# Kernel tuning notes

Measured on AMD Instinct MI355X. Metric: run time of the kernel, lower is better.

Reference implementation:

```python
import jax, jax.numpy as jnp
import numpy as np

NH, HD, WS, LL, SR, HF = 8, 32, 3, 9, 8, 682


def _ln(x, w, b, eps=1e-5):
    m = x.mean(-1, keepdims=True)
    v = ((x - m) ** 2).mean(-1, keepdims=True)
    return (x - m) * jax.lax.rsqrt(v + eps) * w + b


def _l2norm(x, eps=1e-12):
    n = jnp.sqrt(jnp.sum(x * x, axis=-1, keepdims=True))
    return x / jnp.maximum(n, eps)


def setup_inputs() -> dict:
    key = jax.random.key(0)
    ks = jax.random.split(key, 32)
    f32 = jnp.float32
    rn = lambda i, shp, s=0.02: jax.random.normal(ks[i], shp, f32) * s
    B, N, C, T = 8, 3136, 256, 1024
    d = {}
    d['x'] = jax.random.normal(ks[0], (B, N, C), f32)
    d['relative_coords_table'] = jax.random.uniform(ks[1], (T, 2), f32, minval=-1.0, maxval=1.0)
    d['seq_length_scale'] = jnp.ones((1,), f32)
    d['norm1_w'] = jnp.ones((C,), f32); d['norm1_b'] = jnp.zeros((C,), f32)
    d['q_w'] = rn(2, (C, C)); d['q_b'] = rn(3, (C,))
    d['kv_w'] = rn(4, (2 * C, C)); d['kv_b'] = rn(5, (2 * C,))
    d['temperature'] = jnp.full((NH, 1, 1), np.log(np.expm1(1.0 / 0.24)), f32)
    d['query_embedding'] = rn(6, (NH, 1, HD))
    d['relative_pos_bias_local'] = rn(7, (NH, LL), 0.0004)
    d['learnable_tokens'] = rn(8, (NH, HD, LL))
    d['learnable_bias'] = jnp.zeros((NH, 1, LL), f32)
    d['sr_w'] = rn(9, (C, C)); d['sr_b'] = rn(10, (C,))
    d['normp_w'] = jnp.ones((C,), f32); d['normp_b'] = jnp.zeros((C,), f32)
    d['cpb_fc1_w'] = rn(11, (512, 2)); d['cpb_fc1_b'] = rn(12, (512,))
    d['cpb_fc2_w'] = rn(13, (NH, 512)); d['cpb_fc2_b'] = rn(14, (NH,))
    d['proj_w'] = rn(15, (C, C)); d['proj_b'] = rn(16, (C,))
    d['norm2_w'] = jnp.ones((C,), f32); d['norm2_b'] = jnp.zeros((C,), f32)
    d['fc1_w'] = rn(17, (2 * HF, C)); d['fc1_b'] = rn(18, (2 * HF,))
    d['dw_w'] = rn(19, (HF, 1, 3, 3)); d['dw_b'] = rn(20, (HF,))
    d['fc2_w'] = rn(21, (C, HF)); d['fc2_b'] = rn(22, (C,))
    d['relative_pos_index'] = jax.random.randint(ks[23], (N, 49), 0, T)
    d['padding_mask'] = jnp.zeros((N, LL), bool)
    d['H'] = 56
    d['W'] = 56
    return d


def _forward(x, relative_coords_table, seq_length_scale, norm1_w, norm1_b, q_w, q_b, kv_w, kv_b,
             temperature, query_embedding, relative_pos_bias_local, learnable_tokens, learnable_bias,
             sr_w, sr_b, normp_w, normp_b, cpb_fc1_w, cpb_fc1_b, cpb_fc2_w, cpb_fc2_b,
             proj_w, proj_b, norm2_w, norm2_b, fc1_w, fc1_b, dw_w, dw_b, fc2_w, fc2_b,
             relative_pos_index, padding_mask, H, W):
    B, N, C = x.shape
    pH, pW = H // SR, W // SR
    pl = pH * pW
    xn = _ln(x, norm1_w, norm1_b)
    # queries: [B, nh, N, hd], cosine-normalized
    q = (xn @ q_w.T + q_b).reshape(B, N, NH, HD).transpose(0, 2, 1, 3)
    q_norm = _l2norm(q)
    q_scaled = (q_norm + query_embedding) * jax.nn.softplus(temperature) * seq_length_scale
    # local keys/values via unfold (3x3 windows, zero-padded)
    kv = xn @ kv_w.T + kv_b                                   # [B, N, 2C]
    k_l, v_l = jnp.split(kv, 2, axis=-1)
    k_l = _l2norm(k_l.reshape(B, N, NH, HD)).reshape(B, N, C)
    kvl = jnp.concatenate([k_l, v_l], -1).transpose(0, 2, 1).reshape(B, 2 * C, H, W)
    pad = WS // 2
    kvp = jnp.pad(kvl, ((0, 0), (0, 0), (pad, pad), (pad, pad)))
    wins = jnp.stack([kvp[:, :, i:i + H, j:j + W] for i in range(WS) for j in range(WS)], axis=2)
    wins = wins.reshape(B, 2 * NH, HD, LL, N).transpose(0, 1, 4, 2, 3)  # [B, 2nh, N, hd, ll]
    k_loc, v_loc = jnp.split(wins, 2, axis=1)
    attn_local = jnp.einsum('bhnd,bhndl->bhnl', q_scaled, k_loc) + relative_pos_bias_local[None, :, None, :]
    attn_local = jnp.where(padding_mask[None, None], -jnp.inf, attn_local)
    # pooled global branch
    x_ = xn.transpose(0, 2, 1).reshape(B, C, H, W)
    x_ = jax.nn.gelu(jnp.einsum('oc,bchw->bohw', sr_w, x_) + sr_b[None, :, None, None], approximate=False)
    x_ = x_.reshape(B, C, pH, SR, pW, SR).mean(axis=(3, 5))  # adaptive avg pool
    x_ = _ln(x_.reshape(B, C, pl).transpose(0, 2, 1), normp_w, normp_b)
    kvp2 = (x_ @ kv_w.T + kv_b).reshape(B, pl, 2 * NH, HD).transpose(0, 2, 1, 3)
    k_pool, v_pool = jnp.split(kvp2, 2, axis=1)               # [B, nh, pl, hd]
    cpb = jax.nn.relu(relative_coords_table @ cpb_fc1_w.T + cpb_fc1_b) @ cpb_fc2_w.T + cpb_fc2_b
    pool_bias = cpb.T[:, relative_pos_index.reshape(-1)].reshape(NH, N, pl)
    attn_pool = q_scaled @ _l2norm(k_pool).transpose(0, 1, 3, 2) + pool_bias[None]
    # joint softmax over local + pool scores
    attn = jax.nn.softmax(jnp.concatenate([attn_local, attn_pool], -1), axis=-1)
    a_loc, a_pool = attn[..., :LL], attn[..., LL:]
    x_local = jnp.einsum('bhnl,bhndl->bhnd',
                         jnp.einsum('bhnd,hdl->bhnl', q_norm, learnable_tokens) + learnable_bias[None] + a_loc,
                         v_loc)
    x_pool = a_pool @ v_pool
    out = (x_local + x_pool).transpose(0, 2, 1, 3).reshape(B, N, C)
    x = x + (out @ proj_w.T + proj_b)
    # ConvolutionalGLU MLP
    xn2 = _ln(x, norm2_w, norm2_b)
    h = xn2 @ fc1_w.T + fc1_b
    h1, v = jnp.split(h, 2, -1)
    hc = h1.transpose(0, 2, 1).reshape(B, HF, H, W)
    hc = jax.lax.conv_general_dilated(hc, dw_w, (1, 1), 'SAME', feature_group_count=HF,
                                      dimension_numbers=('NCHW', 'OIHW', 'NCHW')) + dw_b[None, :, None, None]
    h1 = hc.reshape(B, HF, N).transpose(0, 2, 1)
    h = jax.nn.gelu(h1, approximate=False) * v
    return x + (h @ fc2_w.T + fc2_b)


def reference(x, relative_coords_table, seq_length_scale, norm1_w, norm1_b, q_w, q_b, kv_w, kv_b,
              temperature, query_embedding, relative_pos_bias_local, learnable_tokens, learnable_bias,
              sr_w, sr_b, normp_w, normp_b, cpb_fc1_w, cpb_fc1_b, cpb_fc2_w, cpb_fc2_b,
              proj_w, proj_b, norm2_w, norm2_b, fc1_w, fc1_b, dw_w, dw_b, fc2_w, fc2_b,
              relative_pos_index, padding_mask, H, W):
    return _forward(x, relative_coords_table, seq_length_scale, norm1_w, norm1_b, q_w, q_b, kv_w, kv_b,
                    temperature, query_embedding, relative_pos_bias_local, learnable_tokens, learnable_bias,
                    sr_w, sr_b, normp_w, normp_b, cpb_fc1_w, cpb_fc1_b, cpb_fc2_w, cpb_fc2_b,
                    proj_w, proj_b, norm2_w, norm2_b, fc1_w, fc1_b, dw_w, dw_b, fc2_w, fc2_b,
                    relative_pos_index, padding_mask, H, W)
```

## Files before the change

### kernel.cpp

```cpp
#include <hip/hip_runtime.h>
#include <math.h>

#define B_   8
#define N_   3136
#define C_   256
#define NH_  8
#define HD_  32
#define LL_  9
#define PL_  49
#define HF_  682
#define HH   56
#define WW   56
#define MROWS (B_*N_)
#define HGLD  704
#define F2LD  704
#define HBLD  1368

typedef short          bf16x8 __attribute__((ext_vector_type(8)));
typedef unsigned short u16x8  __attribute__((ext_vector_type(8)));
typedef float          f32x4  __attribute__((ext_vector_type(4)));
typedef unsigned short u16;

static __device__ __forceinline__ float gelu_f(float x){ return 0.5f*x*(1.0f+erff(x*0.70710678118654752f)); }
static __device__ __forceinline__ u16 f2bf(float f){
// ... 121 lines not shown

  const int Kt = (K + 31) & ~31;
  const int l15 = lane & 15, quad = lane >> 4;
  int r  = tid >> 2;
  int c8 = (tid & 3) * 8;

  for (int k0=0; k0<Kt; k0+=32){
    int gk = k0 + c8;
    u16x8 av = (u16x8){0,0,0,0,0,0,0,0};
    if (m0 + r < M && gk + 8 <= lda)
      av = *(const u16x8*)(A + (size_t)(m0+r)*lda + gk);
    *(u16x8*)(&As[r*LDT + c8]) = av;
    u16x8 bv = (u16x8){0,0,0,0,0,0,0,0};
    if (n0 + r < Nt && gk + 8 <= ldw)
      bv = *(const u16x8*)(W + (size_t)(n0+r)*ldw + gk);
    *(u16x8*)(&Bs[r*LDT + c8]) = bv;
    __syncthreads();
    bf16x8 af[2], bfr[2];
    #pragma unroll
    for (int mi=0;mi<2;mi++)
      af[mi] = *(bf16x8*)(&As[(wm + mi*16 + l15)*LDT + quad*8]);
    #pragma unroll
    for (int nj=0;nj<2;nj++)
      bfr[nj] = *(bf16x8*)(&Bs[(wn + nj*16 + l15)*LDT + quad*8]);
    #pragma unroll
    for (int mi=0;mi<2;mi++)
      #pragma unroll
      for (int nj=0;nj<2;nj++)
        acc[mi][nj] = __builtin_amdgcn_mfma_f32_16x16x32_bf16(af[mi], bfr[nj], acc[mi][nj], 0,0,0);
    __syncthreads();
  }
  int rbase = quad*4;
  #pragma unroll
  for (int nj=0;nj<2;nj++){
    int gc = n0 + wn + nj*16 + l15;
    if (gc >= Nt) continue;
    float bv = bias[gc];
    #pragma unroll
    for (int mi=0;mi<2;mi++){
      #pragma unroll
      for (int reg=0;reg<4;reg++){
        int gr = m0 + wm + mi*16 + rbase + reg;
        if (gr >= M) continue;
        float v = acc[mi][nj][reg] + bv;
        if (ACT==1) v = gelu_f(v);
        if (RES)   v += res[(size_t)gr*Nt + gc];
        if (OUTBF) ((u16*)outv)[(size_t)gr*Nt + gc] = f2bf(v);
        else       ((float*)outv)[(size_t)gr*Nt + gc] = v;
      }
    }
  }
}

__global__ __launch_bounds__(256) void gemm64f(const u16* __restrict__ A,
                                               const u16* __restrict__ W0,
                                               const u16* __restrict__ W1,
                                               const u16* __restrict__ W2,
                                               const float* __restrict__ b0,
                                               const float* __restrict__ b1,
                                               const float* __restrict__ b2,
                                               u16* __restrict__ o0,
                                               u16* __restrict__ o1,
                                               u16* __restrict__ o2){
  constexpr int LDT = 40;
  __shared__ u16 As[64*LDT];
  __shared__ u16 Bs[64*LDT];
  int tid = threadIdx.x, lane = tid & 63;
  int wave = tid >> 6;
  int m0 = blockIdx.x*64, y = blockIdx.y;
  const u16* Wp; const float* bp; u16* dst; int dld, dcol0; bool act = false;
  if (y < 4)      { Wp = W0 + (size_t)y*64*C_;      bp = b0 + y*64;      dst = o0; dld = 256; dcol0 = y*64; }
  else if (y < 12){ Wp = W1 + (size_t)(y-4)*64*C_;  bp = b1 + (y-4)*64;  dst = o1; dld = 512; dcol0 = (y-4)*64; }
  else            { Wp = W2 + (size_t)(y-12)*64*C_; bp = b2 + (y-12)*64; dst = o2; dld = 256; dcol0 = (y-12)*64; act = true; }
  int wm = (wave>>1)*32, wn = (wave&1)*32;
  f32x4 acc[2][2];
  #pragma unroll
  for (int i=0;i<2;i++)
    #pragma unroll
    for (int j=0;j<2;j++) acc[i][j] = (f32x4){0.f,0.f,0.f,0.f};

  const int l15 = lane & 15, quad = lane >> 4;
  int r  = tid >> 2;
  int c8 = (tid & 3) * 8;

  #pragma unroll 1
  for (int k0=0; k0<256; k0+=32){
    int gk = k0 + c8;
    *(u16x8*)(&As[r*LDT + c8]) = *(const u16x8*)(A  + (size_t)(m0+r)*C_ + gk);
    *(u16x8*)(&Bs[r*LDT + c8]) = *(const u16x8*)(Wp + (size_t)r*C_ + gk);
    __syncthreads();
    bf16x8 af[2], bfr[2];
    #pragma unroll
    for (int mi=0;mi<2;mi++)
      af[mi] = *(bf16x8*)(&As[(wm + mi*16 + l15)*LDT + quad*8]);
    #pragma unroll
    for (int nj=0;nj<2;nj++)
      bfr[nj] = *(bf16x8*)(&Bs[(wn + nj*16 + l15)*LDT + quad*8]);
    #pragma unroll
    for (int mi=0;mi<2;mi++)
      #pragma unroll
      for (int nj=0;nj<2;nj++)
        acc[mi][nj] = __builtin_amdgcn_mfma_f32_16x16x32_bf16(af[mi], bfr[nj], acc[mi][nj], 0,0,0);
    __syncthreads();
  }
  int rbase = quad*4;
  #pragma unroll
  for (int nj=0;nj<2;nj++){
    int cc = wn + nj*16 + l15;
    float bv = bp[cc];
    #pragma unroll
    for (int mi=0;mi<2;mi++){
      #pragma unroll
      for (int reg=0;reg<4;reg++){
        int gr = m0 + wm + mi*16 + rbase + reg;
        float v = acc[mi][nj][reg] + bv;
        if (act) v = gelu_f(v);
        dst[(size_t)gr*dld + dcol0 + cc] = f2bf(v);
      }
    }
  }
}

__global__ __launch_bounds__(256) void gemm128a(const u16* __restrict__ A, int lda,
                                                const u16* __restrict__ W, int ldw,
                                                const float* __restrict__ bias,
                                                u16* __restrict__ out,
                                                int M, int Nt, int K, int ldo){
  __shared__ u16 smem[8704];
  u16* As = smem;
  u16* Bs = smem + 4096;
  int tid = threadIdx.x, lane = tid & 63, wave = tid >> 6;
  int m0 = blockIdx.x*128, n0 = blockIdx.y*128;
  int wm = (wave>>1)*64, wn = (wave&1)*64;
  int l15 = lane & 15, quad = lane >> 4;
  f32x4 acc[4][4];
  #pragma unroll
  for (int i=0;i<4;i++)
    #pragma unroll
    for (int j=0;j<4;j++) acc[i][j] = (f32x4){0.f,0.f,0.f,0.f};

  const int Kt = (K + 31) & ~31;
  const u16* ga = A + (size_t)(m0 + lane)*lda + wave*8;
  const u16* gb = W + (size_t)(n0 + lane)*ldw + wave*8;
  u16* la = As + wave*1024;
  u16* lb = Bs + wave*1024;

  for (int k0=0; k0<Kt; k0+=32){
    gld_lds16(ga + k0,            la);
    gld_lds16(ga + 64*lda + k0,   la + 512);
    gld_lds16(gb + k0,            lb);
    gld_lds16(gb + 64*ldw + k0,   lb + 512);
    __syncthreads();
    bf16x8 af[4], bfr[4];
    #pragma unroll
    for (int mi=0;mi<4;mi++)
      af[mi] = *(bf16x8*)(&As[quad*1024 + (wm + mi*16 + l15)*8]);
    #pragma unroll
    for (int nj=0;nj<4;nj++)
      bfr[nj] = *(bf16x8*)(&Bs[quad*1024 + (wn + nj*16 + l15)*8]);
    #pragma unroll
    for (int mi=0;mi<4;mi++)
      #pragma unroll
      for (int nj=0;nj<4;nj++)
        acc[mi][nj] = __builtin_amdgcn_mfma_f32_16x16x32_bf16(af[mi], bfr[nj], acc[mi][nj], 0,0,0);
    __syncthreads();
  }

  u16* Cs = smem;
  #pragma unroll
  for (int p=0;p<2;p++){
    if (wm == p*64){
      #pragma unroll
      for (int nj=0;nj<4;nj++){
        int cc = wn + nj*16 + l15;
        int gc = n0 + cc;
        float bv = (gc < Nt) ? bias[gc] : 0.f;
        #pragma unroll
        for (int mi=0;mi<4;mi++)
          #pragma unroll
          for (int reg=0;reg<4;reg++){
            int rr = mi*16 + quad*4 + reg;
            Cs[rr*136 + cc] = f2bf(acc[mi][nj][reg] + bv);
          }
      }
    }
    __syncthreads();
    int r = tid >> 2, cb = (tid & 3)*32;
    int gr = m0 + p*64 + r;
    if (gr < M){
      u16* op = out + (size_t)gr*ldo + n0;
      #pragma unroll
      for (int k=0;k<4;k++){
        int c0 = cb + k*8;
        if (n0 + c0 + 8 <= ldo)
          *(u16x8*)(op + c0) = *(u16x8*)&Cs[r*136 + c0];
      }
    }
    __syncthreads();
  }
}

__global__ __launch_bounds__(256) void qkpost_kernel(u16* __restrict__ q,
                                                     const float* __restrict__ qe,
                                                     const float* __restrict__ temp,
                                                     const float* __restrict__ sls,
                                                     u16* __restrict__ qs_out,
                                                     u16* __restrict__ kv){
  int row = blockIdx.x, tid = threadIdx.x, h = tid>>5;
  size_t idx = (size_t)row*C_ + tid;
  float v = b2f(q[idx]);
  float ss = rsum32(v*v);
  float qn = v / fmaxf(sqrtf(ss), 1e-12f);
  q[idx] = f2bf(qn);
  float t  = temp[h];
  float sp = log1pf(expf(t));
  float scale = sp * sls[0];
  qs_out[idx] = f2bf((qn + qe[tid])*scale);
  size_t kidx = (size_t)row*512 + tid;
  float kvv = b2f(kv[kidx]);
  float ks = rsum32(kvv*kvv);
  kv[kidx] = f2bf(kvv / fmaxf(sqrtf(ks), 1e-12f));
}

__global__ __launch_bounds__(256) void knorm_kernel(u16* __restrict__ kv){
  int row = blockIdx.x, tid = threadIdx.x;
  size_t idx = (size_t)row*512 + tid;
  float v = b2f(kv[idx]);
  float ss = rsum32(v*v);
  kv[idx] = f2bf(v / fmaxf(sqrtf(ss), 1e-12f));
}

__global__ __launch_bounds__(256) void pool_ln_kernel(const u16* __restrict__ xsr,
                                                      const float* __restrict__ w,
                                                      const float* __restrict__ bsh,
                                                      u16* __restrict__ out){
  int blk = blockIdx.x; int b = blk/PL_; int p = blk%PL_;
  int py = p/7, px = p%7;
  int o = threadIdx.x;
  float s = 0.f;
  for (int iy=0;iy<8;iy++){
    const u16* rowp = xsr + ((size_t)(b*N_ + (py*8+iy)*WW + px*8))*C_ + o;
    #pragma unroll
    for (int ix=0;ix<8;ix++) s += b2f(rowp[(size_t)ix*C_]);
  }
  s *= (1.0f/64.0f);
  float su = rsum64(s), sq = rsum64(s*s);
  __shared__ float s1[4], s2[4];
  if ((o&63)==0){ s1[o>>6]=su; s2[o>>6]=sq; }
  __syncthreads();
  float ts=s1[0]+s1[1]+s1[2]+s1[3];
  float tq=s2[0]+s2[1]+s2[2]+s2[3];
  float m = ts*(1.0f/256.0f), var = tq*(1.0f/256.0f)-m*m;
  float inv = rsqrtf(var+1e-5f);
  out[(size_t)blk*C_+o] = f2bf((s-m)*inv*w[o]+bsh[o]);
}

__global__ __launch_bounds__(256) void cpb_kernel(const float* __restrict__ rct,
                                                  const float* __restrict__ w1,
                                                  const float* __restrict__ b1,
                                                  const float* __restrict__ w2,
                                                  const float* __restrict__ b2v,
                                                  float* __restrict__ cpb){
  __shared__ float r[512];
  int t = blockIdx.x, tid = threadIdx.x;
  float c0 = rct[t*2], c1 = rct[t*2+1];
  for (int j=tid;j<512;j+=256){
    float v = c0*w1[j*2] + c1*w1[j*2+1] + b1[j];
    r[j] = fmaxf(v, 0.f);
  }
  __syncthreads();
  int h = tid>>5, lane = tid&31;
  float s = 0.f;
  for (int j=lane;j<512;j+=32) s += r[j]*w2[h*512+j];
  s = rsum32(s);
  if (lane==0) cpb[t*8+h] = s + b2v[h];
}

__global__ __launch_bounds__(256) void attn_local_v3(const u16* __restrict__ qs,
                                                     const u16* __restrict__ kv,
                                                     const float* __restrict__ rpb,
                                                     float* __restrict__ attn){
  int t = threadIdx.x;
  int row = blockIdx.x*32 + (t>>3);
  int h = t & 7;
  int b = row / N_, n = row - b*N_;
  int y = n / WW, x = n - y*WW;
  const u16* qp = qs + (size_t)row*C_ + h*32;
  float q[32];
  #pragma unroll
  for (int j=0;j<4;j++){
    u16x8 v = *(const u16x8*)(qp + j*8);
    #pragma unroll
    for (int e=0;e<8;e++) q[j*8+e] = b2f(v[e]);
  }
  float* arow = attn + ((size_t)row*8 + h)*58;
  #pragma unroll
  for (int l=0;l<9;l++){
    int yy = y + l/3 - 1, xx = x + l%3 - 1;
    float s = 0.f;
    if (yy>=0 && yy<HH && xx>=0 && xx<WW){
      const u16* kp = kv + ((size_t)(b*N_ + yy*WW + xx))*512 + h*32;
      #pragma unroll
      for (int j=0;j<4;j++){
        u16x8 kw = *(const u16x8*)(kp + j*8);
        #pragma unroll
        for (int e=0;e<8;e++) s = fmaf(q[j*8+e], b2f(kw[e]), s);
      }
    }
    arow[l] = s + rpb[h*9+l];
  }
}

__global__ __launch_bounds__(256) void attn_pool_mfma(const u16* __restrict__ qs,
                                                      const u16* __restrict__ kvp2,
                                                      const float* __restrict__ cpb,
                                                      const int* __restrict__ ridx,
                                                      float* __restrict__ attn){
  int tid = threadIdx.x, lane = tid & 63, wave = tid >> 6;
  int l15 = lane & 15, quad = lane >> 4;
  int bh = blockIdx.y, b = bh >> 3, h = bh & 7;
  int n0 = (blockIdx.x*4 + wave)*16;
  bf16x8 af = *(const bf16x8*)(qs + ((size_t)(b*N_ + n0 + l15)*C_ + h*32 + quad*8));
  f32x4 acc[4];
  #pragma unroll
  for (int nj=0;nj<4;nj++){
    int p = nj*16 + l15;
    bf16x8 bfr = (bf16x8){0,0,0,0,0,0,0,0};
    if (p < PL_)
      bfr = *(const bf16x8*)(kvp2 + ((size_t)(b*PL_ + p)*512 + h*32 + quad*8));
    f32x4 z = (f32x4){0.f,0.f,0.f,0.f};
    acc[nj] = __builtin_amdgcn_mfma_f32_16x16x32_bf16(af, bfr, z, 0,0,0);
  }
  #pragma unroll
  for (int nj=0;nj<4;nj++){
    int p = nj*16 + l15;
    if (p >= PL_) continue;
    #pragma unroll
    for (int reg=0;reg<4;reg++){
      int n = n0 + quad*4 + reg;
      float bias = cpb[ridx[(size_t)n*PL_ + p]*8 + h];
      attn[((size_t)(b*N_ + n)*8 + h)*58 + 9 + p] = acc[nj][reg] + bias;
    }
  }
}

__global__ __launch_bounds__(256) void xout_v4(const float* __restrict__ qlt,
                                               const float* __restrict__ attn,
                                               const u16* __restrict__ kv,
                                               const u16* __restrict__ kvp2,
                                               u16* __restrict__ out){
  __shared__ float coef[4][472];
  int t = threadIdx.x, w = t>>6, l = t&63;
  int row = blockIdx.x*4 + w;
  int b = row / N_, n = row - b*N_;
  int y = n / WW, x = n - y*WW;
  const float* arow = attn + (size_t)row*464;
  for (int i=l; i<464; i+=64) coef[w][i] = arow[i];
  __syncthreads();
  int h = l>>3, k = l&7;
  float* ch = &coef[w][h*58];
  float e[8];
  float mx = -1e30f;
  #pragma unroll
  for (int i=0;i<8;i++){
    int j = k + i*8;
    e[i] = (j<58) ? ch[j] : -1e30f;
    mx = fmaxf(mx, e[i]);
  }
  mx = fmaxf(mx, __shfl_xor(mx,1,64));
  mx = fmaxf(mx, __shfl_xor(mx,2,64));
  mx = fmaxf(mx, __shfl_xor(mx,4,64));
  float s = 0.f;
  #pragma unroll
  for (int i=0;i<8;i++){
    int j = k + i*8;
    if (j<58){ e[i] = expf(e[i]-mx); s += e[i]; }
  }
  s += __shfl_xor(s,1,64);
  s += __shfl_xor(s,2,64);
  s += __shfl_xor(s,4,64);
  float inv = 1.f/s;
  #pragma unroll
  for (int i=0;i<8;i++){
    int j = k + i*8;
    if (j<58){
      float v = e[i]*inv;
      if (j<9) v += qlt[(size_t)row*72 + h*9 + j];
      ch[j] = v;
    }
  }
  __syncthreads();
  int c = l*4;
  float a0=0.f, a1=0.f, a2=0.f, a3=0.f;
  #pragma unroll
  for (int lw=0; lw<9; lw++){
    int yy = y + lw/3 - 1, xx = x + lw%3 - 1;
    if (yy>=0 && yy<HH && xx>=0 && xx<WW){
      ushort4 vv = *(const ushort4*)(kv + ((size_t)(b*N_ + yy*WW + xx))*512 + 256 + c);
      float cf = ch[lw];
      a0 = fmaf(cf, b2f(vv.x), a0);
      a1 = fmaf(cf, b2f(vv.y), a1);
      a2 = fmaf(cf, b2f(vv.z), a2);
      a3 = fmaf(cf, b2f(vv.w), a3);
    }
  }
  const u16* pb = kvp2 + (size_t)b*PL_*512 + 256 + c;
  #pragma unroll 7
  for (int p=0;p<49;p++){
    ushort4 vv = *(const ushort4*)(pb + (size_t)p*512);
    float cf = ch[9+p];
    a0 = fmaf(cf, b2f(vv.x), a0);
    a1 = fmaf(cf, b2f(vv.y), a1);
    a2 = fmaf(cf, b2f(vv.z), a2);
    a3 = fmaf(cf, b2f(vv.w), a3);
  }
  ushort4 o; o.x=f2bf(a0); o.y=f2bf(a1); o.z=f2bf(a2); o.w=f2bf(a3);
  *(ushort4*)(out + (size_t)row*C_ + c) = o;
}

__global__ __launch_bounds__(256) void dwconv_v4(const u16* __restrict__ hsrc,
                                                 const float* __restrict__ dwwT,
                                                 const float* __restrict__ dwb,
                                                 u16* __restrict__ hg){
  int b = blockIdx.x;
  int idx = blockIdx.y*256 + threadIdx.x;
  if (idx >= N_*86) return;
  int n = idx/86, g = idx - n*86;
  int pix = b*N_ + n;
  int y = n / WW, x = n - y*WW;
  const u16* hb = hsrc + (size_t)b*N_*HBLD;
  if (g < 85){
    int f = g*8;
    float s[8];
    #pragma unroll
    for (int e=0;e<8;e++) s[e] = dwb[f+e];
    #pragma unroll
    for (int l=0;l<9;l++){
      int yy = y + l/3 - 1, xx = x + l%3 - 1;
      if (yy>=0 && yy<HH && xx>=0 && xx<WW){
        u16x8 hv = *(const u16x8*)(hb + (size_t)(yy*WW+xx)*HBLD + f);
        const float* wv = dwwT + (size_t)l*684 + f;
        #pragma unroll
        for (int e=0;e<8;e++) s[e] = fmaf(b2f(hv[e]), wv[e], s[e]);
      }
// ... 48 lines not shown
  const float* lb   = (const float*)d_in[13];
  const float* sr_w = (const float*)d_in[14];
  const float* sr_b = (const float*)d_in[15];
  const float* npw  = (const float*)d_in[16];
  const float* npb  = (const float*)d_in[17];
  const float* c1w  = (const float*)d_in[18];
  const float* c1b  = (const float*)d_in[19];
  const float* c2w  = (const float*)d_in[20];
  const float* c2b  = (const float*)d_in[21];
  const float* pw   = (const float*)d_in[22];
  const float* pb   = (const float*)d_in[23];
  const float* n2w  = (const float*)d_in[24];
  const float* n2b  = (const float*)d_in[25];
  const float* f1w  = (const float*)d_in[26];
  const float* f1b  = (const float*)d_in[27];
  const float* dww  = (const float*)d_in[28];
  const float* dwb  = (const float*)d_in[29];
  const float* f2w  = (const float*)d_in[30];
  const float* f2bb = (const float*)d_in[31];
  const int*  ridx  = (const int*)d_in[32];
  float* outp = (float*)d_out;

  char* ws = (char*)d_ws;
  constexpr size_t SZ_BNC2 = (size_t)MROWS*C_*2;
  constexpr size_t SZ_KV2  = (size_t)MROWS*512*2;
  constexpr size_t SZ_ATTN = (size_t)MROWS*464*4;
  size_t o_xn   = 0;
  size_t o_qn   = o_xn   + SZ_BNC2;
  size_t o_qs   = o_qn   + SZ_BNC2;
  size_t o_kv   = o_qs   + SZ_BNC2;
  size_t o_attn = o_kv   + SZ_KV2;
  size_t o_xsr  = o_attn + SZ_ATTN;
  size_t o_xpln = o_xsr  + SZ_BNC2;
  size_t o_kvp2 = o_xpln + (size_t)B_*PL_*C_*2;
  size_t o_cpb  = o_kvp2 + (size_t)B_*PL_*512*2;
  size_t o_outb = o_cpb  + (size_t)1024*8*4;
  size_t o_x2   = o_outb + SZ_BNC2;
  size_t o_qlt  = o_x2   + (size_t)MROWS*C_*4;
  size_t o_wq   = o_qlt  + (size_t)MROWS*72*4;
  size_t o_wkv  = o_wq   + (size_t)65536*2;
  size_t o_wsr  = o_wkv  + (size_t)131072*2;
  size_t o_wp   = o_wsr  + (size_t)65536*2;
  size_t o_wf1  = o_wp   + (size_t)65536*2;
  size_t o_wf2  = o_wf1  + (size_t)360448*2;
  size_t o_w72  = o_wf2  + (size_t)256*F2LD*2;
  size_t o_dwwT = o_w72  + (size_t)72*256*2;
  size_t o_h    = o_kv;
  size_t o_hg   = 0;

  u16*   xn   = (u16*)(ws + o_xn);
  u16*   qbuf = (u16*)(ws + o_qn);
  u16*   qsc  = (u16*)(ws + o_qs);
  u16*   kv   = (u16*)(ws + o_kv);
  float* attn = (float*)(ws + o_attn);
  u16*   xsr  = (u16*)(ws + o_xsr);
  u16*   xpln = (u16*)(ws + o_xpln);
  u16*   kvp2 = (u16*)(ws + o_kvp2);
  float* cpb  = (float*)(ws + o_cpb);
  u16*   outb = (u16*)(ws + o_outb);
  float* x2   = (float*)(ws + o_x2);
  float* qlt  = (float*)(ws + o_qlt);
  u16*   wq   = (u16*)(ws + o_wq);
  u16*   wkv  = (u16*)(ws + o_wkv);
  u16*   wsr  = (u16*)(ws + o_wsr);
  u16*   wp   = (u16*)(ws + o_wp);
  u16*   wf1  = (u16*)(ws + o_wf1);
  u16*   wf2  = (u16*)(ws + o_wf2);
  u16*   w72  = (u16*)(ws + o_w72);
  float* dwwT = (float*)(ws + o_dwwT);
  u16*   hbuf = (u16*)(ws + o_h);
  u16*   hg   = (u16*)(ws + o_hg);

  cvt_all<<<dim3(64,8), 256, 0, stream>>>(q_w, kv_w, sr_w, pw, f1w, f2w, lt, dww,
                                          wq, wkv, wsr, wp, wf1, wf2, w72, dwwT);
  ln_kernel<<<MROWS, 256, 0, stream>>>(x, n1w, n1b, xn);
  gemm64f<<<dim3(392,16), 256, 0, stream>>>(xn, wq, wkv, wsr, q_b, kv_b, sr_b,
                                            qbuf, kv, xsr);
  qkpost_kernel<<<MROWS, 256, 0, stream>>>(qbuf, qe, temp, sls, qsc, kv);
  pool_ln_kernel<<<B_*PL_, 256, 0, stream>>>(xsr, npw, npb, xpln);
  gemm64b<0,0,1><<<dim3(7,8), 256, 0, stream>>>(xpln, C_, wkv, C_, kv_b, nullptr, kvp2, B_*PL_, 512, 256);
  knorm_kernel<<<B_*PL_, 256, 0, stream>>>(kvp2);
  cpb_kernel<<<1024, 256, 0, stream>>>(rct, c1w, c1b, c2w, c2b, cpb);
  gemm64b<0,0,0><<<dim3(392,2), 256, 0, stream>>>(qbuf, C_, w72, C_, lb, nullptr, qlt, MROWS, 72, 256);
  attn_local_v3<<<MROWS/32, 256, 0, stream>>>(qsc, kv, rpb, attn);
  attn_pool_mfma<<<dim3(49,64), 256, 0, stream>>>(qsc, kvp2, cpb, ridx, attn);
  xout_v4<<<MROWS/4, 256, 0, stream>>>(qlt, attn, kv, kvp2, outb);
  gemm64b<0,1,0><<<dim3(392,4), 256, 0, stream>>>(outb, C_, wp, C_, pb, x, x2, MROWS, 256, 256);
  ln_kernel<<<MROWS, 256, 0, stream>>>(x2, n2w, n2b, xn);
  gemm128a<<<dim3(196,11), 256, 0, stream>>>(xn, C_, wf1, C_, f1b, hbuf, MROWS, 1364, 256, HBLD);
  dwconv_v4<<<dim3(8, (N_*86+255)/256), 256, 0, stream>>>(hbuf, dwwT, dwb, hg);
  gemm64b<0,1,0><<<dim3(392,4), 256, 0, stream>>>(hg, HGLD, wf2, F2LD, f2bb, x2, outp, MROWS, 256, HF_);
}
```

Before: 571.3 us.

## Fuse local and pooled attention score computation into the softmax/output kernel

Removes the separate attn_local and attn_pool_mfma kernels and computes the local and pooled q·k scores directly inside the output kernel, so the per-row fp32 attention buffer is no longer written and read back. Each thread loads its head's query into registers and computes up to 8 dot products with scalar FMAs. The pooled scores move from MFMA to scalar FMAs and each lane now holds 32 query values in registers, which may raise register pressure and compute cost.

```diff
diff --git a/kernel.cpp b/kernel.cpp
--- a/kernel.cpp
+++ b/kernel.cpp
@@ -421,97 +421,66 @@
   if (lane==0) cpb[t*8+h] = s + b2v[h];
 }
 
-__global__ __launch_bounds__(256) void attn_local_v3(const u16* __restrict__ qs,
-                                                     const u16* __restrict__ kv,
-                                                     const float* __restrict__ rpb,
-                                                     float* __restrict__ attn){
-  int t = threadIdx.x;
-  int row = blockIdx.x*32 + (t>>3);
-  int h = t & 7;
-  int b = row / N_, n = row - b*N_;
-  int y = n / WW, x = n - y*WW;
-  const u16* qp = qs + (size_t)row*C_ + h*32;
-  float q[32];
-  #pragma unroll
-  for (int j=0;j<4;j++){
-    u16x8 v = *(const u16x8*)(qp + j*8);
-    #pragma unroll
-    for (int e=0;e<8;e++) q[j*8+e] = b2f(v[e]);
-  }
-  float* arow = attn + ((size_t)row*8 + h)*58;
-  #pragma unroll
-  for (int l=0;l<9;l++){
-    int yy = y + l/3 - 1, xx = x + l%3 - 1;
-    float s = 0.f;
-    if (yy>=0 && yy<HH && xx>=0 && xx<WW){
-      const u16* kp = kv + ((size_t)(b*N_ + yy*WW + xx))*512 + h*32;
-      #pragma unroll
-      for (int j=0;j<4;j++){
-        u16x8 kw = *(const u16x8*)(kp + j*8);
-        #pragma unroll
-        for (int e=0;e<8;e++) s = fmaf(q[j*8+e], b2f(kw[e]), s);
-      }
-    }
-    arow[l] = s + rpb[h*9+l];
-  }
-}
-
-__global__ __launch_bounds__(256) void attn_pool_mfma(const u16* __restrict__ qs,
-                                                      const u16* __restrict__ kvp2,
-                                                      const float* __restrict__ cpb,
-                                                      const int* __restrict__ ridx,
-                                                      float* __restrict__ attn){
-  int tid = threadIdx.x, lane = tid & 63, wave = tid >> 6;
-  int l15 = lane & 15, quad = lane >> 4;
-  int bh = blockIdx.y, b = bh >> 3, h = bh & 7;
-  int n0 = (blockIdx.x*4 + wave)*16;
-  bf16x8 af = *(const bf16x8*)(qs + ((size_t)(b*N_ + n0 + l15)*C_ + h*32 + quad*8));
-  f32x4 acc[4];
-  #pragma unroll
-  for (int nj=0;nj<4;nj++){
-    int p = nj*16 + l15;
-    bf16x8 bfr = (bf16x8){0,0,0,0,0,0,0,0};
-    if (p < PL_)
-      bfr = *(const bf16x8*)(kvp2 + ((size_t)(b*PL_ + p)*512 + h*32 + quad*8));
-    f32x4 z = (f32x4){0.f,0.f,0.f,0.f};
-    acc[nj] = __builtin_amdgcn_mfma_f32_16x16x32_bf16(af, bfr, z, 0,0,0);
-  }
-  #pragma unroll
-  for (int nj=0;nj<4;nj++){
-    int p = nj*16 + l15;
-    if (p >= PL_) continue;
-    #pragma unroll
-    for (int reg=0;reg<4;reg++){
-      int n = n0 + quad*4 + reg;
-      float bias = cpb[ridx[(size_t)n*PL_ + p]*8 + h];
-      attn[((size_t)(b*N_ + n)*8 + h)*58 + 9 + p] = acc[nj][reg] + bias;
-    }
-  }
-}
-
-__global__ __launch_bounds__(256) void xout_v4(const float* __restrict__ qlt,
-                                               const float* __restrict__ attn,
+__global__ __launch_bounds__(256) void xout_v5(const float* __restrict__ qlt,
+                                               const u16* __restrict__ qsc,
                                                const u16* __restrict__ kv,
                                                const u16* __restrict__ kvp2,
+                                               const float* __restrict__ cpb,
+                                               const int* __restrict__ ridx,
+                                               const float* __restrict__ rpb,
                                                u16* __restrict__ out){
   __shared__ float coef[4][472];
   int t = threadIdx.x, w = t>>6, l = t&63;
   int row = blockIdx.x*4 + w;
   int b = row / N_, n = row - b*N_;
   int y = n / WW, x = n - y*WW;
-  const float* arow = attn + (size_t)row*464;
-  for (int i=l; i<464; i+=64) coef[w][i] = arow[i];
-  __syncthreads();
   int h = l>>3, k = l&7;
-  float* ch = &coef[w][h*58];
+
+  float q[32];
+  const u16* qp = qsc + (size_t)row*C_ + h*32;
+  #pragma unroll
+  for (int j=0;j<4;j++){
+    u16x8 v = *(const u16x8*)(qp + j*8);
+    #pragma unroll
+    for (int e8=0;e8<8;e8++) q[j*8+e8] = b2f(v[e8]);
+  }
+
   float e[8];
-  float mx = -1e30f;
   #pragma unroll
   for (int i=0;i<8;i++){
     int j = k + i*8;
-    e[i] = (j<58) ? ch[j] : -1e30f;
-    mx = fmaxf(mx, e[i]);
-  }
+    float s = -1e30f;
+    if (j < 9){
+      int yy = y + j/3 - 1, xx = x + j%3 - 1;
+      s = 0.f;
+      if (yy>=0 && yy<HH && xx>=0 && xx<WW){
+        const u16* kp = kv + ((size_t)(b*N_ + yy*WW + xx))*512 + h*32;
+        #pragma unroll
+        for (int jj=0;jj<4;jj++){
+          u16x8 kw = *(const u16x8*)(kp + jj*8);
+          #pragma unroll
+          for (int ee=0;ee<8;ee++) s = fmaf(q[jj*8+ee], b2f(kw[ee]), s);
+        }
+      }
+      s += rpb[h*9+j];
+    } else if (j < 58){
+      int p = j - 9;
+      const u16* kp = kvp2 + ((size_t)(b*PL_ + p))*512 + h*32;
+      float d = 0.f;
+      #pragma unroll
+      for (int jj=0;jj<4;jj++){
+        u16x8 kw = *(const u16x8*)(kp + jj*8);
+        #pragma unroll
+        for (int ee=0;ee<8;ee++) d = fmaf(q[jj*8+ee], b2f(kw[ee]), d);
+      }
+      s = d + cpb[ridx[(size_t)n*PL_ + p]*8 + h];
+    }
+    e[i] = s;
+  }
+
+  float mx = -1e30f;
+  #pragma unroll
+  for (int i=0;i<8;i++) mx = fmaxf(mx, e[i]);
   mx = fmaxf(mx, __shfl_xor(mx,1,64));
   mx = fmaxf(mx, __shfl_xor(mx,2,64));
   mx = fmaxf(mx, __shfl_xor(mx,4,64));
@@ -525,6 +494,7 @@
   s += __shfl_xor(s,2,64);
   s += __shfl_xor(s,4,64);
   float inv = 1.f/s;
+  float* ch = &coef[w][h*58];
   #pragma unroll
   for (int i=0;i<8;i++){
     int j = k + i*8;
@@ -535,6 +505,7 @@
     }
   }
   __syncthreads();
+
   int c = l*4;
   float a0=0.f, a1=0.f, a2=0.f, a3=0.f;
   #pragma unroll
@@ -689,7 +660,6 @@
   u16*   qbuf = (u16*)(ws + o_qn);
   u16*   qsc  = (u16*)(ws + o_qs);
   u16*   kv   = (u16*)(ws + o_kv);
-  float* attn = (float*)(ws + o_attn);
   u16*   xsr  = (u16*)(ws + o_xsr);
   u16*   xpln = (u16*)(ws + o_xpln);
   u16*   kvp2 = (u16*)(ws + o_kvp2);
@@ -719,9 +689,7 @@
   knorm_kernel<<<B_*PL_, 256, 0, stream>>>(kvp2);
   cpb_kernel<<<1024, 256, 0, stream>>>(rct, c1w, c1b, c2w, c2b, cpb);
   gemm64b<0,0,0><<<dim3(392,2), 256, 0, stream>>>(qbuf, C_, w72, C_, lb, nullptr, qlt, MROWS, 72, 256);
-  attn_local_v3<<<MROWS/32, 256, 0, stream>>>(qsc, kv, rpb, attn);
-  attn_pool_mfma<<<dim3(49,64), 256, 0, stream>>>(qsc, kvp2, cpb, ridx, attn);
-  xout_v4<<<MROWS/4, 256, 0, stream>>>(qlt, attn, kv, kvp2, outb);
+  xout_v5<<<MROWS/4, 256, 0, stream>>>(qlt, qsc, kv, kvp2, cpb, ridx, rpb, outb);
   gemm64b<0,1,0><<<dim3(392,4), 256, 0, stream>>>(outb, C_, wp, C_, pb, x, x2, MROWS, 256, 256);
   ln_kernel<<<MROWS, 256, 0, stream>>>(x2, n2w, n2b, xn);
   gemm128a<<<dim3(196,11), 256, 0, stream>>>(xn, C_, wf1, C_, f1b, hbuf, MROWS, 1364, 256, HBLD);
```

Measured after the change: 605.3 us. +5.9%, slower.

## Use 128x128 tiles for fused QKV/SR GEMM and merge small kernels

Applied to the files above, without the earlier changes.

The 64x64-tile fused q/kv/sr projection GEMM is replaced by a templated 128x128-tile kernel with direct global-to-LDS loads. The same template also serves the fc1 GEMM. Several small kernels are merged into multi-role launches selected by block index: q/k post-processing with pool+LN, k-norm with the CPB MLP, and the qlt GEMM with the local and pooled attention scores. The aim is more operand reuse per tile and fewer launches and gaps between kernels. In exchange, the merged kernels mix block types with different resource needs, and the larger GEMM tile launches fewer blocks.

```diff
diff --git a/kernel.cpp b/kernel.cpp
--- a/kernel.cpp
+++ b/kernel.cpp
@@ -197,87 +197,37 @@
   }
 }
 
-__global__ __launch_bounds__(256) void gemm64f(const u16* __restrict__ A,
-                                               const u16* __restrict__ W0,
-                                               const u16* __restrict__ W1,
-                                               const u16* __restrict__ W2,
-                                               const float* __restrict__ b0,
-                                               const float* __restrict__ b1,
-                                               const float* __restrict__ b2,
-                                               u16* __restrict__ o0,
-                                               u16* __restrict__ o1,
-                                               u16* __restrict__ o2){
-  constexpr int LDT = 40;
-  __shared__ u16 As[64*LDT];
-  __shared__ u16 Bs[64*LDT];
-  int tid = threadIdx.x, lane = tid & 63;
-  int wave = tid >> 6;
-  int m0 = blockIdx.x*64, y = blockIdx.y;
-  const u16* Wp; const float* bp; u16* dst; int dld, dcol0; bool act = false;
-  if (y < 4)      { Wp = W0 + (size_t)y*64*C_;      bp = b0 + y*64;      dst = o0; dld = 256; dcol0 = y*64; }
-  else if (y < 12){ Wp = W1 + (size_t)(y-4)*64*C_;  bp = b1 + (y-4)*64;  dst = o1; dld = 512; dcol0 = (y-4)*64; }
-  else            { Wp = W2 + (size_t)(y-12)*64*C_; bp = b2 + (y-12)*64; dst = o2; dld = 256; dcol0 = (y-12)*64; act = true; }
-  int wm = (wave>>1)*32, wn = (wave&1)*32;
-  f32x4 acc[2][2];
-  #pragma unroll
-  for (int i=0;i<2;i++)
-    #pragma unroll
-    for (int j=0;j<2;j++) acc[i][j] = (f32x4){0.f,0.f,0.f,0.f};
-
-  const int l15 = lane & 15, quad = lane >> 4;
-  int r  = tid >> 2;
-  int c8 = (tid & 3) * 8;
-
-  #pragma unroll 1
-  for (int k0=0; k0<256; k0+=32){
-    int gk = k0 + c8;
-    *(u16x8*)(&As[r*LDT + c8]) = *(const u16x8*)(A  + (size_t)(m0+r)*C_ + gk);
-    *(u16x8*)(&Bs[r*LDT + c8]) = *(const u16x8*)(Wp + (size_t)r*C_ + gk);
-    __syncthreads();
-    bf16x8 af[2], bfr[2];
-    #pragma unroll
-    for (int mi=0;mi<2;mi++)
-      af[mi] = *(bf16x8*)(&As[(wm + mi*16 + l15)*LDT + quad*8]);
-    #pragma unroll
-    for (int nj=0;nj<2;nj++)
-      bfr[nj] = *(bf16x8*)(&Bs[(wn + nj*16 + l15)*LDT + quad*8]);
-    #pragma unroll
-    for (int mi=0;mi<2;mi++)
-      #pragma unroll
-      for (int nj=0;nj<2;nj++)
-        acc[mi][nj] = __builtin_amdgcn_mfma_f32_16x16x32_bf16(af[mi], bfr[nj], acc[mi][nj], 0,0,0);
-    __syncthreads();
-  }
-  int rbase = quad*4;
-  #pragma unroll
-  for (int nj=0;nj<2;nj++){
-    int cc = wn + nj*16 + l15;
-    float bv = bp[cc];
-    #pragma unroll
-    for (int mi=0;mi<2;mi++){
-      #pragma unroll
-      for (int reg=0;reg<4;reg++){
-        int gr = m0 + wm + mi*16 + rbase + reg;
-        float v = acc[mi][nj][reg] + bv;
-        if (act) v = gelu_f(v);
-        dst[(size_t)gr*dld + dcol0 + cc] = f2bf(v);
-      }
-    }
-  }
-}
-
-__global__ __launch_bounds__(256) void gemm128a(const u16* __restrict__ A, int lda,
-                                                const u16* __restrict__ W, int ldw,
-                                                const float* __restrict__ bias,
-                                                u16* __restrict__ out,
+template<int EPI>
+__global__ __launch_bounds__(256) void gemm128t(const u16* __restrict__ A, int lda,
+                                                const u16* __restrict__ W0,
+                                                const u16* __restrict__ W1,
+                                                const u16* __restrict__ W2,
+                                                const float* __restrict__ b0,
+                                                const float* __restrict__ b1,
+                                                const float* __restrict__ b2,
+                                                u16* __restrict__ o0,
+                                                u16* __restrict__ o1,
+                                                u16* __restrict__ o2,
                                                 int M, int Nt, int K, int ldo){
   __shared__ u16 smem[8704];
   u16* As = smem;
   u16* Bs = smem + 4096;
   int tid = threadIdx.x, lane = tid & 63, wave = tid >> 6;
-  int m0 = blockIdx.x*128, n0 = blockIdx.y*128;
+  int m0 = blockIdx.x*128, y = blockIdx.y;
   int wm = (wave>>1)*64, wn = (wave&1)*64;
   int l15 = lane & 15, quad = lane >> 4;
+
+  const u16* Wp; const float* bp; u16* dstb; int dld, dcol0; bool act = false;
+  if (EPI==2){
+    if (y < 2){      Wp = W0 + (size_t)y*128*C_;     bp = b0 + y*128;     dstb = o0; dld = 256; dcol0 = y*128; }
+    else if (y < 6){ Wp = W1 + (size_t)(y-2)*128*C_; bp = b1 + (y-2)*128; dstb = o1; dld = 512; dcol0 = (y-2)*128; }
+    else {           Wp = W2 + (size_t)(y-6)*128*C_; bp = b2 + (y-6)*128; dstb = o2; dld = 256; dcol0 = (y-6)*128; act = true; }
+  } else {
+    Wp = W0 + (size_t)y*128*(size_t)lda; bp = b0; dstb = o0; dld = ldo; dcol0 = y*128;
+  }
+  const int ldwv = (EPI==2) ? C_ : lda;
+  const int ldav = (EPI==2) ? C_ : lda;
+
   f32x4 acc[4][4];
   #pragma unroll
   for (int i=0;i<4;i++)
@@ -285,16 +235,16 @@
     for (int j=0;j<4;j++) acc[i][j] = (f32x4){0.f,0.f,0.f,0.f};
 
   const int Kt = (K + 31) & ~31;
-  const u16* ga = A + (size_t)(m0 + lane)*lda + wave*8;
-  const u16* gb = W + (size_t)(n0 + lane)*ldw + wave*8;
+  const u16* ga = A  + (size_t)(m0 + lane)*ldav + wave*8;
+  const u16* gb = Wp + (size_t)lane*ldwv + wave*8;
   u16* la = As + wave*1024;
   u16* lb = Bs + wave*1024;
 
   for (int k0=0; k0<Kt; k0+=32){
-    gld_lds16(ga + k0,            la);
-    gld_lds16(ga + 64*lda + k0,   la + 512);
-    gld_lds16(gb + k0,            lb);
-    gld_lds16(gb + 64*ldw + k0,   lb + 512);
+    gld_lds16(ga + k0,              la);
+    gld_lds16(ga + 64*ldav + k0,    la + 512);
+    gld_lds16(gb + k0,              lb);
+    gld_lds16(gb + 64*ldwv + k0,    lb + 512);
     __syncthreads();
     bf16x8 af[4], bfr[4];
     #pragma unroll
@@ -318,173 +268,238 @@
       #pragma unroll
       for (int nj=0;nj<4;nj++){
         int cc = wn + nj*16 + l15;
-        int gc = n0 + cc;
-        float bv = (gc < Nt) ? bias[gc] : 0.f;
+        float bv;
+        if (EPI==0){ int gc = dcol0 + cc; bv = (gc < Nt) ? bp[gc] : 0.f; }
+        else       { bv = bp[cc]; }
         #pragma unroll
-        for (int mi=0;mi<4;mi++)
+        for (int mi=0;mi<4;mi++){
           #pragma unroll
           for (int reg=0;reg<4;reg++){
             int rr = mi*16 + quad*4 + reg;
-            Cs[rr*136 + cc] = f2bf(acc[mi][nj][reg] + bv);
+            float v = acc[mi][nj][reg] + bv;
+            if (act) v = gelu_f(v);
+            Cs[rr*136 + cc] = f2bf(v);
           }
+        }
       }
     }
     __syncthreads();
     int r = tid >> 2, cb = (tid & 3)*32;
     int gr = m0 + p*64 + r;
     if (gr < M){
-      u16* op = out + (size_t)gr*ldo + n0;
+      u16* op = dstb + (size_t)gr*dld + dcol0;
       #pragma unroll
       for (int k=0;k<4;k++){
         int c0 = cb + k*8;
-        if (n0 + c0 + 8 <= ldo)
-          *(u16x8*)(op + c0) = *(u16x8*)&Cs[r*136 + c0];
+        bool ok = (EPI==0) ? (dcol0 + c0 + 8 <= ldo) : true;
+        if (ok) *(u16x8*)(op + c0) = *(u16x8*)&Cs[r*136 + c0];
       }
     }
     __syncthreads();
   }
 }
 
-__global__ __launch_bounds__(256) void qkpost_kernel(u16* __restrict__ q,
-                                                     const float* __restrict__ qe,
-                                                     const float* __restrict__ temp,
-                                                     const float* __restrict__ sls,
-                                                     u16* __restrict__ qs_out,
-                                                     u16* __restrict__ kv){
-  int row = blockIdx.x, tid = threadIdx.x, h = tid>>5;
-  size_t idx = (size_t)row*C_ + tid;
-  float v = b2f(q[idx]);
-  float ss = rsum32(v*v);
-  float qn = v / fmaxf(sqrtf(ss), 1e-12f);
-  q[idx] = f2bf(qn);
-  float t  = temp[h];
-  float sp = log1pf(expf(t));
-  float scale = sp * sls[0];
-  qs_out[idx] = f2bf((qn + qe[tid])*scale);
-  size_t kidx = (size_t)row*512 + tid;
-  float kvv = b2f(kv[kidx]);
-  float ks = rsum32(kvv*kvv);
-  kv[kidx] = f2bf(kvv / fmaxf(sqrtf(ks), 1e-12f));
-}
-
-__global__ __launch_bounds__(256) void knorm_kernel(u16* __restrict__ kv){
-  int row = blockIdx.x, tid = threadIdx.x;
-  size_t idx = (size_t)row*512 + tid;
-  float v = b2f(kv[idx]);
-  float ss = rsum32(v*v);
-  kv[idx] = f2bf(v / fmaxf(sqrtf(ss), 1e-12f));
-}
-
-__global__ __launch_bounds__(256) void pool_ln_kernel(const u16* __restrict__ xsr,
-                                                      const float* __restrict__ w,
-                                                      const float* __restrict__ bsh,
-                                                      u16* __restrict__ out){
-  int blk = blockIdx.x; int b = blk/PL_; int p = blk%PL_;
-  int py = p/7, px = p%7;
-  int o = threadIdx.x;
-  float s = 0.f;
-  for (int iy=0;iy<8;iy++){
-    const u16* rowp = xsr + ((size_t)(b*N_ + (py*8+iy)*WW + px*8))*C_ + o;
-    #pragma unroll
-    for (int ix=0;ix<8;ix++) s += b2f(rowp[(size_t)ix*C_]);
-  }
-  s *= (1.0f/64.0f);
-  float su = rsum64(s), sq = rsum64(s*s);
+__global__ __launch_bounds__(256) void post1_kernel(u16* __restrict__ q,
+                                                    const float* __restrict__ qe,
+                                                    const float* __restrict__ temp,
+                                                    const float* __restrict__ sls,
+                                                    u16* __restrict__ qs_out,
+                                                    u16* __restrict__ kv,
+                                                    const u16* __restrict__ xsr,
+                                                    const float* __restrict__ npw,
+                                                    const float* __restrict__ npb,
+                                                    u16* __restrict__ xpln){
   __shared__ float s1[4], s2[4];
-  if ((o&63)==0){ s1[o>>6]=su; s2[o>>6]=sq; }
-  __syncthreads();
-  float ts=s1[0]+s1[1]+s1[2]+s1[3];
-  float tq=s2[0]+s2[1]+s2[2]+s2[3];
-  float m = ts*(1.0f/256.0f), var = tq*(1.0f/256.0f)-m*m;
-  float inv = rsqrtf(var+1e-5f);
-  out[(size_t)blk*C_+o] = f2bf((s-m)*inv*w[o]+bsh[o]);
-}
-
-__global__ __launch_bounds__(256) void cpb_kernel(const float* __restrict__ rct,
-                                                  const float* __restrict__ w1,
-                                                  const float* __restrict__ b1,
-                                                  const float* __restrict__ w2,
-                                                  const float* __restrict__ b2v,
-                                                  float* __restrict__ cpb){
+  int bid = blockIdx.x, tid = threadIdx.x;
+  if (bid < MROWS){
+    int row = bid, h = tid>>5;
+    size_t idx = (size_t)row*C_ + tid;
+    float v = b2f(q[idx]);
+    float ss = rsum32(v*v);
+    float qn = v / fmaxf(sqrtf(ss), 1e-12f);
+    q[idx] = f2bf(qn);
+    float t  = temp[h];
+    float sp = log1pf(expf(t));
+    float scale = sp * sls[0];
+    qs_out[idx] = f2bf((qn + qe[tid])*scale);
+    size_t kidx = (size_t)row*512 + tid;
+    float kvv = b2f(kv[kidx]);
+    float ks = rsum32(kvv*kvv);
+    kv[kidx] = f2bf(kvv / fmaxf(sqrtf(ks), 1e-12f));
+  } else {
+    int blk = bid - MROWS;
+    int b = blk/PL_; int p = blk%PL_;
+    int py = p/7, px = p%7;
+    int o = tid;
+    float s = 0.f;
+    for (int iy=0;iy<8;iy++){
+      const u16* rowp = xsr + ((size_t)(b*N_ + (py*8+iy)*WW + px*8))*C_ + o;
+      #pragma unroll
+      for (int ix=0;ix<8;ix++) s += b2f(rowp[(size_t)ix*C_]);
+    }
+    s *= (1.0f/64.0f);
+    float su = rsum64(s), sq = rsum64(s*s);
+    if ((o&63)==0){ s1[o>>6]=su; s2[o>>6]=sq; }
+    __syncthreads();
+    float ts=s1[0]+s1[1]+s1[2]+s1[3];
+    float tq=s2[0]+s2[1]+s2[2]+s2[3];
+    float m = ts*(1.0f/256.0f), var = tq*(1.0f/256.0f)-m*m;
+    float inv = rsqrtf(var+1e-5f);
+    xpln[(size_t)blk*C_+o] = f2bf((s-m)*inv*npw[o]+npb[o]);
+  }
+}
+
+__global__ __launch_bounds__(256) void misc2_kernel(u16* __restrict__ kvp2,
+                                                    const float* __restrict__ rct,
+                                                    const float* __restrict__ w1,
+                                                    const float* __restrict__ b1,
+                                                    const float* __restrict__ w2,
+                                                    const float* __restrict__ b2v,
+                                                    float* __restrict__ cpb){
   __shared__ float r[512];
-  int t = blockIdx.x, tid = threadIdx.x;
-  float c0 = rct[t*2], c1 = rct[t*2+1];
-  for (int j=tid;j<512;j+=256){
-    float v = c0*w1[j*2] + c1*w1[j*2+1] + b1[j];
-    r[j] = fmaxf(v, 0.f);
-  }
-  __syncthreads();
-  int h = tid>>5, lane = tid&31;
-  float s = 0.f;
-  for (int j=lane;j<512;j+=32) s += r[j]*w2[h*512+j];
-  s = rsum32(s);
-  if (lane==0) cpb[t*8+h] = s + b2v[h];
-}
-
-__global__ __launch_bounds__(256) void attn_local_v3(const u16* __restrict__ qs,
-                                                     const u16* __restrict__ kv,
-                                                     const float* __restrict__ rpb,
-                                                     float* __restrict__ attn){
-  int t = threadIdx.x;
-  int row = blockIdx.x*32 + (t>>3);
-  int h = t & 7;
-  int b = row / N_, n = row - b*N_;
-  int y = n / WW, x = n - y*WW;
-  const u16* qp = qs + (size_t)row*C_ + h*32;
-  float q[32];
-  #pragma unroll
-  for (int j=0;j<4;j++){
-    u16x8 v = *(const u16x8*)(qp + j*8);
-    #pragma unroll
-    for (int e=0;e<8;e++) q[j*8+e] = b2f(v[e]);
-  }
-  float* arow = attn + ((size_t)row*8 + h)*58;
-  #pragma unroll
-  for (int l=0;l<9;l++){
-    int yy = y + l/3 - 1, xx = x + l%3 - 1;
+  int bid = blockIdx.x, tid = threadIdx.x;
+  if (bid < B_*PL_){
+    int row = bid;
+    size_t idx = (size_t)row*512 + tid;
+    float v = b2f(kvp2[idx]);
+    float ss = rsum32(v*v);
+    kvp2[idx] = f2bf(v / fmaxf(sqrtf(ss), 1e-12f));
+  } else {
+    int t = bid - B_*PL_;
+    float c0 = rct[t*2], c1 = rct[t*2+1];
+    for (int j=tid;j<512;j+=256){
+      float v = c0*w1[j*2] + c1*w1[j*2+1] + b1[j];
+      r[j] = fmaxf(v, 0.f);
+    }
+    __syncthreads();
+    int h = tid>>5, lane = tid&31;
     float s = 0.f;
-    if (yy>=0 && yy<HH && xx>=0 && xx<WW){
-      const u16* kp = kv + ((size_t)(b*N_ + yy*WW + xx))*512 + h*32;
-      #pragma unroll
-      for (int j=0;j<4;j++){
-        u16x8 kw = *(const u16x8*)(kp + j*8);
+    for (int j=lane;j<512;j+=32) s += r[j]*w2[h*512+j];
+    s = rsum32(s);
+    if (lane==0) cpb[t*8+h] = s + b2v[h];
+  }
+}
+
+__global__ __launch_bounds__(256) void attn_all(const u16* __restrict__ qbuf,
+                                                const u16* __restrict__ w72,
+                                                const float* __restrict__ lb,
+                                                float* __restrict__ qlt,
+                                                const u16* __restrict__ qs,
+                                                const u16* __restrict__ kv,
+                                                const float* __restrict__ rpb,
+                                                const u16* __restrict__ kvp2,
+                                                const float* __restrict__ cpb,
+                                                const int* __restrict__ ridx,
+                                                float* __restrict__ attn){
+  constexpr int LDT = 40;
+  __shared__ u16 As[64*LDT];
+  __shared__ u16 Bs[64*LDT];
+  int bid = blockIdx.x, tid = threadIdx.x;
+  int lane = tid & 63, wave = tid >> 6;
+  int l15 = lane & 15, quad = lane >> 4;
+  if (bid < 784){
+    int m0 = (bid % 392)*64, n0 = (bid / 392)*64;
+    int wm = (wave>>1)*32, wn = (wave&1)*32;
+    f32x4 acc[2][2];
+    #pragma unroll
+    for (int i=0;i<2;i++)
+      #pragma unroll
+      for (int j=0;j<2;j++) acc[i][j] = (f32x4){0.f,0.f,0.f,0.f};
+    int r  = tid >> 2;
+    int c8 = (tid & 3) * 8;
+    for (int k0=0; k0<256; k0+=32){
+      int gk = k0 + c8;
+      *(u16x8*)(&As[r*LDT + c8]) = *(const u16x8*)(qbuf + (size_t)(m0+r)*C_ + gk);
+      u16x8 bv = (u16x8){0,0,0,0,0,0,0,0};
+      if (n0 + r < 72)
+        bv = *(const u16x8*)(w72 + (size_t)(n0+r)*C_ + gk);
+      *(u16x8*)(&Bs[r*LDT + c8]) = bv;
+      __syncthreads();
+      bf16x8 af[2], bfr[2];
+      #pragma unroll
+      for (int mi=0;mi<2;mi++)
+        af[mi] = *(bf16x8*)(&As[(wm + mi*16 + l15)*LDT + quad*8]);
+      #pragma unroll
+      for (int nj=0;nj<2;nj++)
+        bfr[nj] = *(bf16x8*)(&Bs[(wn + nj*16 + l15)*LDT + quad*8]);
+      #pragma unroll
+      for (int mi=0;mi<2;mi++)
         #pragma unroll
-        for (int e=0;e<8;e++) s = fmaf(q[j*8+e], b2f(kw[e]), s);
+        for (int nj=0;nj<2;nj++)
+          acc[mi][nj] = __builtin_amdgcn_mfma_f32_16x16x32_bf16(af[mi], bfr[nj], acc[mi][nj], 0,0,0);
+      __syncthreads();
+    }
+    int rbase = quad*4;
+    #pragma unroll
+    for (int nj=0;nj<2;nj++){
+      int gc = n0 + wn + nj*16 + l15;
+      if (gc >= 72) continue;
+      float bv = lb[gc];
+      #pragma unroll
+      for (int mi=0;mi<2;mi++){
+        #pragma unroll
+        for (int reg=0;reg<4;reg++){
+          int gr = m0 + wm + mi*16 + rbase + reg;
+          qlt[(size_t)gr*72 + gc] = acc[mi][nj][reg] + bv;
+        }
       }
     }
-    arow[l] = s + rpb[h*9+l];
-  }
-}
-
-__global__ __launch_bounds__(256) void attn_pool_mfma(const u16* __restrict__ qs,
-                                                      const u16* __restrict__ kvp2,
-                                                      const float* __restrict__ cpb,
-                                                      const int* __restrict__ ridx,
-                                                      float* __restrict__ attn){
-  int tid = threadIdx.x, lane = tid & 63, wave = tid >> 6;
-  int l15 = lane & 15, quad = lane >> 4;
-  int bh = blockIdx.y, b = bh >> 3, h = bh & 7;
-  int n0 = (blockIdx.x*4 + wave)*16;
-  bf16x8 af = *(const bf16x8*)(qs + ((size_t)(b*N_ + n0 + l15)*C_ + h*32 + quad*8));
-  f32x4 acc[4];
-  #pragma unroll
-  for (int nj=0;nj<4;nj++){
-    int p = nj*16 + l15;
-    bf16x8 bfr = (bf16x8){0,0,0,0,0,0,0,0};
-    if (p < PL_)
-      bfr = *(const bf16x8*)(kvp2 + ((size_t)(b*PL_ + p)*512 + h*32 + quad*8));
-    f32x4 z = (f32x4){0.f,0.f,0.f,0.f};
-    acc[nj] = __builtin_amdgcn_mfma_f32_16x16x32_bf16(af, bfr, z, 0,0,0);
-  }
-  #pragma unroll
-  for (int nj=0;nj<4;nj++){
-    int p = nj*16 + l15;
-    if (p >= PL_) continue;
-    #pragma unroll
-    for (int reg=0;reg<4;reg++){
-      int n = n0 + quad*4 + reg;
-      float bias = cpb[ridx[(size_t)n*PL_ + p]*8 + h];
-      attn[((size_t)(b*N_ + n)*8 + h)*58 + 9 + p] = acc[nj][reg] + bias;
+  } else if (bid < 1568){
+    int t = tid;
+    int row = (bid-784)*32 + (t>>3);
+    int h = t & 7;
+    int b = row / N_, n = row - b*N_;
+    int y = n / WW, x = n - y*WW;
+    const u16* qp = qs + (size_t)row*C_ + h*32;
+    float q[32];
+    #pragma unroll
+    for (int j=0;j<4;j++){
+      u16x8 v = *(const u16x8*)(qp + j*8);
+      #pragma unroll
+      for (int e=0;e<8;e++) q[j*8+e] = b2f(v[e]);
+    }
+    float* arow = attn + ((size_t)row*8 + h)*58;
+    #pragma unroll
+    for (int l=0;l<9;l++){
+      int yy = y + l/3 - 1, xx = x + l%3 - 1;
+      float s = 0.f;
+      if (yy>=0 && yy<HH && xx>=0 && xx<WW){
+        const u16* kp = kv + ((size_t)(b*N_ + yy*WW + xx))*512 + h*32;
+        #pragma unroll
+        for (int j=0;j<4;j++){
+          u16x8 kw = *(const u16x8*)(kp + j*8);
+          #pragma unroll
+          for (int e=0;e<8;e++) s = fmaf(q[j*8+e], b2f(kw[e]), s);
+        }
+      }
+      arow[l] = s + rpb[h*9+l];
+    }
+  } else {
+    int t = bid - 1568;
+    int xblk = t % 49, bh = t / 49;
+    int b = bh >> 3, h = bh & 7;
+    int n0 = (xblk*4 + wave)*16;
+    bf16x8 af = *(const bf16x8*)(qs + ((size_t)(b*N_ + n0 + l15)*C_ + h*32 + quad*8));
+    f32x4 acc[4];
+    #pragma unroll
+    for (int nj=0;nj<4;nj++){
+      int p = nj*16 + l15;
+      bf16x8 bfr = (bf16x8){0,0,0,0,0,0,0,0};
+      if (p < PL_)
+        bfr = *(const bf16x8*)(kvp2 + ((size_t)(b*PL_ + p)*512 + h*32 + quad*8));
+      f32x4 z = (f32x4){0.f,0.f,0.f,0.f};
+      acc[nj] = __builtin_amdgcn_mfma_f32_16x16x32_bf16(af, bfr, z, 0,0,0);
+    }
+    #pragma unroll
+    for (int nj=0;nj<4;nj++){
+      int p = nj*16 + l15;
+      if (p >= PL_) continue;
+      #pragma unroll
+      for (int reg=0;reg<4;reg++){
+        int n = n0 + quad*4 + reg;
+        float bias = cpb[ridx[(size_t)n*PL_ + p]*8 + h];
+        attn[((size_t)(b*N_ + n)*8 + h)*58 + 9 + p] = acc[nj][reg] + bias;
+      }
     }
   }
 }
@@ -711,20 +726,19 @@
   cvt_all<<<dim3(64,8), 256, 0, stream>>>(q_w, kv_w, sr_w, pw, f1w, f2w, lt, dww,
                                           wq, wkv, wsr, wp, wf1, wf2, w72, dwwT);
   ln_kernel<<<MROWS, 256, 0, stream>>>(x, n1w, n1b, xn);
-  gemm64f<<<dim3(392,16), 256, 0, stream>>>(xn, wq, wkv, wsr, q_b, kv_b, sr_b,
-                                            qbuf, kv, xsr);
-  qkpost_kernel<<<MROWS, 256, 0, stream>>>(qbuf, qe, temp, sls, qsc, kv);
-  pool_ln_kernel<<<B_*PL_, 256, 0, stream>>>(xsr, npw, npb, xpln);
+  gemm128t<2><<<dim3(196,8), 256, 0, stream>>>(xn, C_, wq, wkv, wsr, q_b, kv_b, sr_b,
+                                               qbuf, kv, xsr, MROWS, 1024, 256, 0);
+  post1_kernel<<<MROWS + B_*PL_, 256, 0, stream>>>(qbuf, qe, temp, sls, qsc, kv,
+                                                   xsr, npw, npb, xpln);
   gemm64b<0,0,1><<<dim3(7,8), 256, 0, stream>>>(xpln, C_, wkv, C_, kv_b, nullptr, kvp2, B_*PL_, 512, 256);
-  knorm_kernel<<<B_*PL_, 256, 0, stream>>>(kvp2);
-  cpb_kernel<<<1024, 256, 0, stream>>>(rct, c1w, c1b, c2w, c2b, cpb);
-  gemm64b<0,0,0><<<dim3(392,2), 256, 0, stream>>>(qbuf, C_, w72, C_, lb, nullptr, qlt, MROWS, 72, 256);
-  attn_local_v3<<<MROWS/32, 256, 0, stream>>>(qsc, kv, rpb, attn);
-  attn_pool_mfma<<<dim3(49,64), 256, 0, stream>>>(qsc, kvp2, cpb, ridx, attn);
+  misc2_kernel<<<B_*PL_ + 1024, 256, 0, stream>>>(kvp2, rct, c1w, c1b, c2w, c2b, cpb);
+  attn_all<<<784 + 784 + 3136, 256, 0, stream>>>(qbuf, w72, lb, qlt,
+                                                 qsc, kv, rpb, kvp2, cpb, ridx, attn);
   xout_v4<<<MROWS/4, 256, 0, stream>>>(qlt, attn, kv, kvp2, outb);
   gemm64b<0,1,0><<<dim3(392,4), 256, 0, stream>>>(outb, C_, wp, C_, pb, x, x2, MROWS, 256, 256);
   ln_kernel<<<MROWS, 256, 0, stream>>>(x2, n2w, n2b, xn);
-  gemm128a<<<dim3(196,11), 256, 0, stream>>>(xn, C_, wf1, C_, f1b, hbuf, MROWS, 1364, 256, HBLD);
+  gemm128t<0><<<dim3(196,11), 256, 0, stream>>>(xn, C_, wf1, nullptr, nullptr, f1b, nullptr, nullptr,
+                                                hbuf, nullptr, nullptr, MROWS, 1364, 256, HBLD);
   dwconv_v4<<<dim3(8, (N_*86+255)/256), 256, 0, stream>>>(hbuf, dwwT, dwb, hg);
   gemm64b<0,1,0><<<dim3(392,4), 256, 0, stream>>>(hg, HGLD, wf2, F2LD, f2bb, x2, outp, MROWS, 256, HF_);
 }
```

New measurement: 594.9 us. +4.1%, slower.
